# Kernel tuning notes

Hardware: AMD Instinct MI355X
Metric: run time of the kernel (lower is better)

## Reference

```python
import jax, jax.numpy as jnp
import numpy as np

N_NODES = 50000
N_EDGES = 800000
IN_F = 128
OUT_F = 32
HEADS = 4
EDGE_F = 32  # must equal OUT_F for the original module's shapes to broadcast


def setup_inputs() -> dict:
    key = jax.random.key(0)
    k1, k2, k3, k4, k5, k6, k7 = jax.random.split(key, 7)
    h = jax.random.normal(k1, (N_NODES, IN_F), dtype=jnp.float32)
    edge_indices = jax.random.randint(k2, (2, N_EDGES), 0, N_NODES, dtype=jnp.int32)
    edge_attr = jax.random.normal(k3, (N_EDGES, EDGE_F), dtype=jnp.float32)
    # learned parameters (xavier-ish scaling)
    W = jax.random.normal(k4, (IN_F, HEADS * OUT_F), dtype=jnp.float32) * (1.0 / np.sqrt(IN_F))
    a = jax.random.normal(k5, (HEADS, 2 * OUT_F + EDGE_F), dtype=jnp.float32) * 0.1
    eW = jax.random.normal(k6, (EDGE_F, HEADS * OUT_F), dtype=jnp.float32) * (1.0 / np.sqrt(EDGE_F))
    eb = jnp.zeros((HEADS * OUT_F,), dtype=jnp.float32)
    return {"h": h, "edge_indices": edge_indices, "edge_attr": edge_attr,
            "W": W, "a": a, "eW": eW, "eb": eb}


def reference(h, edge_indices, edge_attr, W, a, eW, eb):
    N = h.shape[0]
    H = a.shape[0]
    F = W.shape[1] // H
    row, col = edge_indices[0], edge_indices[1]

    # node / edge projections
    ht = (h @ W).reshape(N, H, F)                       # [N,H,F]
    et = (edge_attr @ eW + eb).reshape(-1, H, F)        # [E,H,F]

    # split attention vector; avoids materializing the [E,H,3F] concat
    a_i, a_j, a_e = a[:, :F], a[:, F:2 * F], a[:, 2 * F:]
    alpha_i = jnp.einsum('nhf,hf->nh', ht, a_i)         # [N,H]
    alpha_j = jnp.einsum('nhf,hf->nh', ht, a_j)         # [N,H]
    e = alpha_i[row] + alpha_j[col] + jnp.einsum('ehf,hf->eh', et, a_e)  # [E,H]
    e = jax.nn.leaky_relu(e, negative_slope=0.2)

    # scatter-softmax over edges grouped by destination (row), global-max stabilized
    e_exp = jnp.exp(e - jnp.max(e))                     # matches torch exp(e - e.max())
    denom = jax.ops.segment_sum(e_exp, row, num_segments=N)  # [N,H]
    att = e_exp / (denom[row] + 1e-8)                   # [E,H]

    # weighted scatter-add aggregation
    hj = ht[col]                                        # [E,H,F]
    h_out = jax.ops.segment_sum(att[:, :, None] * hj, row, num_segments=N)  # [N,H,F]
    h_out = h_out.reshape(N, H * F)                     # concat=True
    h_out = jax.nn.elu(h_out)                           # dropout=0 (eval)
    return h_out, att
```

## Files before the change

### kernel.cpp

```cpp
#include <hip/hip_runtime.h>
#include <hip/hip_bf16.h>
#include <hip/hip_fp16.h>

#define N_NODES 50000
#define N_EDGES 800000
#define IN_F 128
#define OUT_F 32
#define HEADS 4
#define EDGE_F 32
#define HF 128
#define SB 256
#define NBLK ((N_NODES + SB - 1) / SB)

typedef __attribute__((ext_vector_type(8))) short short8_t;
typedef __attribute__((ext_vector_type(4))) float f32x4;

__device__ __forceinline__ unsigned short f2bf(float x) {
    unsigned int u = __float_as_uint(x);
    unsigned int r = (u + 0x7FFF + ((u >> 16) & 1)) >> 16;
    return (unsigned short)r;
}
__device__ __forceinline__ float bf2f(unsigned short b) {
    return __uint_as_float(((unsigned int)b) << 16);
}

__global__ void prep_kernel(const float* __restrict__ eW, const float* __restrict__ eb,
                            const float* __restrict__ a,
                            float* __restrict__ w_eff, float* __restrict__ b_eff) {
    int t = threadIdx.x;
    if (t < 128) {
        int k = t >> 2, h = t & 3;
        float s = 0.f;
        #pragma unroll
        for (int f = 0; f < EDGE_F; ++f)
            s = fmaf(eW[k * HF + h * OUT_F + f], a[h * 96 + 2 * OUT_F + f], s);
        w_eff[k * 4 + h] = s;
    } else if (t < 132) {
        int h = t - 128;
        float s = 0.f;
        #pragma unroll
        for (int f = 0; f < EDGE_F; ++f)
            s = fmaf(eb[h * OUT_F + f], a[h * 96 + 2 * OUT_F + f], s);
        b_eff[h] = s;
    }
}

__global__ __launch_bounds__(256) void prepW_kernel(const float* __restrict__ W,
                                                    unsigned short* __restrict__ W_T) {
    int g = blockIdx.x * 256 + threadIdx.x;
    int n = g >> 4, c = g & 15;
    unsigned short w8[8];
    #pragma unroll
    for (int q = 0; q < 8; ++q)
        w8[q] = f2bf(W[(size_t)(8 * c + q) * 128 + n]);
    *(uint4*)&W_T[n * 128 + ((c ^ (n & 7)) << 3)] = *(uint4*)w8;
}

__global__ __launch_bounds__(256) void node_kernel(
        const float* __restrict__ h, const unsigned short* __restrict__ W_T,
        const float* __restrict__ a,
        __hip_bfloat16* __restrict__ ht_bf,
        float* __restrict__ alpha_i, float* __restrict__ alpha_j) {
    __shared__ __align__(16) unsigned short Wl[128 * 128];
    __shared__ __align__(16) unsigned short Hhi[64 * 128];
    __shared__ __align__(16) unsigned short Hlo[64 * 128];
    int t = threadIdx.x;
    int lane = t & 63, wave = t >> 6;
    int nb = blockIdx.x * 64;
    {
        const uint4* src = (const uint4*)W_T;
        uint4* dst = (uint4*)Wl;
        #pragma unroll
        for (int u = 0; u < 8; ++u) dst[t + u * 256] = src[t + u * 256];
    }
    #pragma unroll
    for (int u = 0; u < 8; ++u) {
        int f = u * 256 + t;
        int row = f >> 5, q = f & 31;
        int gn = nb + row; if (gn > N_NODES - 1) gn = N_NODES - 1;
        float4 v = ((const float4*)h)[(size_t)gn * 32 + q];
        unsigned short hi[4], lo[4];
        #pragma unroll
        for (int x = 0; x < 4; ++x) {
            float xv = (&v.x)[x];
            unsigned short hb = f2bf(xv);
            hi[x] = hb;
            lo[x] = f2bf(xv - bf2f(hb));
        }
        int c = q >> 1, half = q & 1;
        int off = row * 128 + ((c ^ (row & 7)) << 3) + half * 4;
        *(uint2*)&Hhi[off] = *(uint2*)hi;
        *(uint2*)&Hlo[off] = *(uint2*)lo;
    }
    __syncthreads();
    int n0 = nb + wave * 16;
    if (n0 >= N_NODES) return;
    int r = lane & 15, g = lane >> 4;
    short8_t ahi[4], alo[4];
    #pragma unroll
    for (int k = 0; k < 4; ++k) {
        int c = k * 4 + g;
        int off = (wave * 16 + r) * 128 + ((c ^ (r & 7)) << 3);
        ahi[k] = *(const short8_t*)&Hhi[off];
        alo[k] = *(const short8_t*)&Hlo[off];
    }
    f32x4 acc[8];
    #pragma unroll
    for (int i = 0; i < 8; ++i) acc[i] = (f32x4){0.f, 0.f, 0.f, 0.f};
    #pragma unroll
    for (int tt = 0; tt < 8; ++tt) {
        int n = tt * 16 + r;
        #pragma unroll
        for (int k = 0; k < 4; ++k) {
            int c = k * 4 + g;
            short8_t b = *(const short8_t*)&Wl[n * 128 + ((c ^ (n & 7)) << 3)];
            acc[tt] = __builtin_amdgcn_mfma_f32_16x16x32_bf16(ahi[k], b, acc[tt], 0, 0, 0);
            acc[tt] = __builtin_amdgcn_mfma_f32_16x16x32_bf16(alo[k], b, acc[tt], 0, 0, 0);
        }
    }
    #pragma unroll
    for (int tt = 0; tt < 8; ++tt)
        #pragma unroll
        for (int reg = 0; reg < 4; ++reg) {
            int rowg = n0 + 4 * g + reg;
            ((unsigned short*)ht_bf)[(size_t)rowg * 128 + tt * 16 + r] = f2bf(acc[tt][reg]);
        }
    float pi[4][4], pj[4][4];
    #pragma unroll
    for (int hh = 0; hh < 4; ++hh) {
        float ai0 = a[hh * 96 + r],      ai1 = a[hh * 96 + 16 + r];
        float aj0 = a[hh * 96 + 32 + r], aj1 = a[hh * 96 + 48 + r];
        #pragma unroll
        for (int reg = 0; reg < 4; ++reg) {
            float v0 = acc[2 * hh][reg], v1 = acc[2 * hh + 1][reg];
            pi[hh][reg] = fmaf(v0, ai0, v1 * ai1);
            pj[hh][reg] = fmaf(v0, aj0, v1 * aj1);
        }
    }
    #pragma unroll
    for (int hh = 0; hh < 4; ++hh)
        #pragma unroll
        for (int reg = 0; reg < 4; ++reg) {
            float vi = pi[hh][reg], vj = pj[hh][reg];
            #pragma unroll
            for (int s = 1; s < 16; s <<= 1) {
                vi += __shfl_xor(vi, s, 64);
                vj += __shfl_xor(vj, s, 64);
            }
            pi[hh][reg] = vi; pj[hh][reg] = vj;
        }
    if (r == 0) {
        #pragma unroll
        for (int hh = 0; hh < 4; ++hh)
            #pragma unroll
            for (int reg = 0; reg < 4; ++reg) {
                int rowg = n0 + 4 * g + reg;
                alpha_i[rowg * 4 + hh] = pi[hh][reg];
                alpha_j[rowg * 4 + hh] = pj[hh][reg];
            }
    }
}

__global__ __launch_bounds__(256) void count_kernel(const int* __restrict__ row,
                                                    int* __restrict__ deg,
                                                    int* __restrict__ rank) {
    int t = blockIdx.x * 256 + threadIdx.x;
    if (t < N_EDGES / 4) {
        int4 r4 = ((const int4*)row)[t];
        int4 k4;
        k4.x = atomicAdd(&deg[r4.x], 1);
        k4.y = atomicAdd(&deg[r4.y], 1);
        k4.z = atomicAdd(&deg[r4.z], 1);
        k4.w = atomicAdd(&deg[r4.w], 1);
        ((int4*)rank)[t] = k4;
    }
}

__device__ __forceinline__ int block_incl_scan(int v, int lane, int wid, int* wsum) {
    int x = v;
    #pragma unroll
    for (int s = 1; s < 64; s <<= 1) {
        int y = __shfl_up(x, s, 64);
        if (lane >= s) x += y;
    }
    if (lane == 63) wsum[wid] = x;
    __syncthreads();
    int add = 0;
    #pragma unroll
    for (int w = 0; w < 4; ++w) add += (w < wid) ? wsum[w] : 0;
    return x + add;
}

__global__ __launch_bounds__(SB) void scan1_kernel(const int* __restrict__ deg,
                                                   int* __restrict__ row_off,
                                                   int* __restrict__ blk_sums) {
    __shared__ int wsum[4];
    int i = blockIdx.x * SB + threadIdx.x;
    int v = (i < N_NODES) ? deg[i] : 0;
    int incl = block_incl_scan(v, threadIdx.x & 63, threadIdx.x >> 6, wsum);
    if (i < N_NODES) row_off[i] = incl - v;
    if (threadIdx.x == SB - 1) blk_sums[blockIdx.x] = incl;
}

__global__ __launch_bounds__(SB) void scan2_kernel(int* __restrict__ blk_sums,
                                                   int* __restrict__ blk_off,
                                                   int* __restrict__ row_off) {
    __shared__ int wsum[4];
    int t = threadIdx.x;
    int v = (t < NBLK) ? blk_sums[t] : 0;
    int incl = block_incl_scan(v, t & 63, t >> 6, wsum);
    if (t < NBLK) blk_off[t] = incl - v;
    if (t == SB - 1) row_off[N_NODES] = incl;
}

__global__ __launch_bounds__(SB) void scan3_kernel(const int* __restrict__ blk_off,
                                                   int* __restrict__ row_off,
                                                   const float* __restrict__ alpha_i,
                                                   float4* __restrict__ nrec) {
    int i = blockIdx.x * SB + threadIdx.x;
    if (i < N_NODES) {
        int v = row_off[i] + blk_off[blockIdx.x];
        row_off[i] = v;
        float4 ai = *(const float4*)(alpha_i + (size_t)i * 4);
        nrec[(size_t)i * 2] = ai;
        float4 m;
        m.x = __int_as_float(v); m.y = 0.f; m.z = 0.f; m.w = 0.f;
        nrec[(size_t)i * 2 + 1] = m;
    }
}

__global__ __launch_bounds__(256) void edge_kernel(
        const int* __restrict__ row, const int* __restrict__ col,
        const int* __restrict__ rank,
        const float* __restrict__ ea,
        const float* __restrict__ w_eff, const float* __restrict__ b_eff,
        const float4* __restrict__ nrec, const float* __restrict__ alpha_j,
        uint4* __restrict__ rec, float4* __restrict__ att_ex) {
    __shared__ __align__(16) float eas[256 * 36];
    __shared__ float wsd[128];
    __shared__ float bs[4];
    int t = threadIdx.x;
    if (t < 128) wsd[t] = w_eff[t];
    if (t < 4) bs[t] = b_eff[t];
    int e0 = blockIdx.x * 256;
    {
        const float4* src = (const float4*)ea + (size_t)e0 * 8;
        #pragma unroll
        for (int u = 0; u < 8; ++u) {
            int f = u * 256 + t;
            int el = f >> 3, j = f & 7;
            *(float4*)&eas[el * 36 + 4 * j] = src[f];
        }
    }
    __syncthreads();
    int e = e0 + t;
    float4 ev[8];
    #pragma unroll
    for (int i = 0; i < 8; ++i) ev[i] = *(const float4*)&eas[t * 36 + 4 * i];
    int r = row[e], c = col[e];
    int rk = rank[e];
    f32x4 ai = ((const f32x4*)nrec)[(size_t)r * 2];
    int ro = ((const int*)nrec)[(size_t)r * 8 + 4];
    f32x4 aj = *(const f32x4*)(alpha_j + (size_t)c * 4);
    float s0 = bs[0], s1 = bs[1], s2 = bs[2], s3 = bs[3];
    #pragma unroll
    for (int i = 0; i < 8; ++i) {
        #pragma unroll
        for (int kk = 0; kk < 4; ++kk) {
            float x = (&ev[i].x)[kk];
            float4 w4 = *(const float4*)&wsd[(i * 4 + kk) * 4];
            s0 = fmaf(x, w4.x, s0);
            s1 = fmaf(x, w4.y, s1);
            s2 = fmaf(x, w4.z, s2);
            s3 = fmaf(x, w4.w, s3);
        }
    }
    float e0v = s0 + ai[0] + aj[0];
    float e1v = s1 + ai[1] + aj[1];
    float e2v = s2 + ai[2] + aj[2];
    float e3v = s3 + ai[3] + aj[3];
    e0v = e0v > 0.f ? e0v : 0.2f * e0v;
    e1v = e1v > 0.f ? e1v : 0.2f * e1v;
    e2v = e2v > 0.f ? e2v : 0.2f * e2v;
    e3v = e3v > 0.f ? e3v : 0.2f * e3v;
    float x0 = __expf(e0v), x1 = __expf(e1v), x2 = __expf(e2v), x3 = __expf(e3v);
    att_ex[e] = make_float4(x0, x1, x2, x3);
    __half2 p01 = __floats2half2_rn(x0, x1);
    __half2 p23 = __floats2half2_rn(x2, x3);
    uint4 o;
    o.x = *reinterpret_cast<unsigned int*>(&p01);
    o.y = *reinterpret_cast<unsigned int*>(&p23);
    o.z = (unsigned int)c;
    o.w = 0u;
    rec[ro + rk] = o;
}

__global__ __launch_bounds__(256) void agg_kernel(
        const int* __restrict__ row_off, const uint4* __restrict__ rec,
        const __hip_bfloat16* __restrict__ ht_bf,
        float* __restrict__ hout, float* __restrict__ rden_buf) {
    int wave = threadIdx.x >> 6;
    int lane = threadIdx.x & 63;
    int n = blockIdx.x * 4 + wave;
    if (n >= N_NODES) return;
    int beg = row_off[n], end = row_off[n + 1];
    int h2 = lane >> 4;
    int sh = (h2 & 1) * 16;
    float2 acc0 = {0.f, 0.f}, acc1 = {0.f, 0.f};
    float den0 = 0.f, den1 = 0.f;
    int p = beg;
    for (; p + 3 < end; p += 4) {
        uint4 rA = rec[p];
        uint4 rB = rec[p + 1];
        uint4 rC = rec[p + 2];
        uint4 rD = rec[p + 3];
        unsigned int wA = (h2 & 2) ? rA.y : rA.x;
        unsigned int wB = (h2 & 2) ? rB.y : rB.x;
        unsigned int wC = (h2 & 2) ? rC.y : rC.x;
        unsigned int wD = (h2 & 2) ? rD.y : rD.x;
        float exA = __half2float(__ushort_as_half((unsigned short)(wA >> sh)));
        float exB = __half2float(__ushort_as_half((unsigned short)(wB >> sh)));
        float exC = __half2float(__ushort_as_half((unsigned short)(wC >> sh)));
        float exD = __half2float(__ushort_as_half((unsigned short)(wD >> sh)));
        float2 hvA = __bfloat1622float2(
            *(const __hip_bfloat162*)(ht_bf + (size_t)rA.z * HF + 2 * lane));
        float2 hvB = __bfloat1622float2(
            *(const __hip_bfloat162*)(ht_bf + (size_t)rB.z * HF + 2 * lane));
        float2 hvC = __bfloat1622float2(
            *(const __hip_bfloat162*)(ht_bf + (size_t)rC.z * HF + 2 * lane));
        float2 hvD = __bfloat1622float2(
            *(const __hip_bfloat162*)(ht_bf + (size_t)rD.z * HF + 2 * lane));
        acc0.x = fmaf(exA, hvA.x, acc0.x); acc0.y = fmaf(exA, hvA.y, acc0.y);
        acc1.x = fmaf(exB, hvB.x, acc1.x); acc1.y = fmaf(exB, hvB.y, acc1.y);
        acc0.x = fmaf(exC, hvC.x, acc0.x); acc0.y = fmaf(exC, hvC.y, acc0.y);
        acc1.x = fmaf(exD, hvD.x, acc1.x); acc1.y = fmaf(exD, hvD.y, acc1.y);
        den0 += exA + exC; den1 += exB + exD;
    }
    for (; p < end; ++p) {
        uint4 rA = rec[p];
        unsigned int wA = (h2 & 2) ? rA.y : rA.x;
        float exA = __half2float(__ushort_as_half((unsigned short)(wA >> sh)));
        float2 hvA = __bfloat1622float2(
            *(const __hip_bfloat162*)(ht_bf + (size_t)rA.z * HF + 2 * lane));
        acc0.x = fmaf(exA, hvA.x, acc0.x); acc0.y = fmaf(exA, hvA.y, acc0.y);
        den0 += exA;
    }
    float den = den0 + den1;
    float rden = 1.0f / (den + 1e-8f);
    float ox = (acc0.x + acc1.x) * rden, oy = (acc0.y + acc1.y) * rden;
    ox = ox > 0.f ? ox : expm1f(ox);
    oy = oy > 0.f ? oy : expm1f(oy);
    float2 o = {ox, oy};
    ((float2*)(hout + (size_t)n * HF))[lane] = o;
    if ((lane & 15) == 0)
        rden_buf[n * 4 + h2] = rden;
}

__global__ __launch_bounds__(256) void norm_kernel(const int* __restrict__ row,
                                                   const float* __restrict__ rden_buf,
                                                   float* __restrict__ att) {
    int e = blockIdx.x * 256 + threadIdx.x;
    float4 ex = ((const float4*)att)[e];
    int r = row[e];
    float4 rd = *(const float4*)(rden_buf + (size_t)r * 4);
    ex.x *= rd.x; ex.y *= rd.y; ex.z *= rd.z; ex.w *= rd.w;
    ((float4*)att)[e] = ex;
}

extern "C" void kernel_launch(void* const* d_in, const int* in_sizes, int n_in,
                              void* d_out, int out_size, void* d_ws, size_t ws_size,
                              hipStream_t stream) {
    const float* h  = (const float*)d_in[0];
    const int*   ei = (const int*)  d_in[1];
    const float* ea = (const float*)d_in[2];
    const float* W  = (const float*)d_in[3];
    const float* a  = (const float*)d_in[4];
    const float* eW = (const float*)d_in[5];
    const float* eb = (const float*)d_in[6];

    float* out  = (float*)d_out;
    float* hout = out;
    float* att  = out + (size_t)N_NODES * HF;

    char* wsb = (char*)d_ws;
    __hip_bfloat16* ht_bf = (__hip_bfloat16*)wsb;
    float* alpha_i = (float*)(wsb + (size_t)N_NODES * HF * 2);
    float* alpha_j = alpha_i + N_NODES * HEADS;
    float* w_eff   = alpha_j + N_NODES * HEADS;
    float* b_eff   = w_eff + 128;
    unsigned short* W_T = (unsigned short*)(b_eff + 4);
    int*   deg     = (int*)(W_T + 128 * 128);
    int*   row_off = deg + N_NODES;
    int*   blk_sums= row_off + N_NODES + 1;
    int*   blk_off = blk_sums + NBLK;
    int*   rank    = (int*)((((uintptr_t)(blk_off + NBLK)) + 15) & ~(uintptr_t)15);
    uint4* rec     = (uint4*)((((uintptr_t)(rank + N_EDGES)) + 15) & ~(uintptr_t)15);
    float* rden_buf= (float*)(rec + N_EDGES);
    float4* nrec   = (float4*)(rden_buf + N_NODES * 4);

    const int* row = ei;
    const int* col = ei + N_EDGES;

    (void)hipMemsetAsync(deg, 0, (size_t)N_NODES * sizeof(int), stream);

    prep_kernel<<<1, 160, 0, stream>>>(eW, eb, a, w_eff, b_eff);
    prepW_kernel<<<8, 256, 0, stream>>>(W, W_T);
    node_kernel<<<(N_NODES + 63) / 64, 256, 0, stream>>>(h, W_T, a, ht_bf, alpha_i, alpha_j);
    count_kernel<<<(N_EDGES / 4 + 255) / 256, 256, 0, stream>>>(row, deg, rank);
    scan1_kernel<<<NBLK, SB, 0, stream>>>(deg, row_off, blk_sums);
    scan2_kernel<<<1, SB, 0, stream>>>(blk_sums, blk_off, row_off);
    scan3_kernel<<<NBLK, SB, 0, stream>>>(blk_off, row_off, alpha_i, nrec);
    edge_kernel<<<N_EDGES / 256, 256, 0, stream>>>(row, col, rank, ea, w_eff, b_eff,
                                                   nrec, alpha_j, rec, (float4*)att);
    agg_kernel<<<(N_NODES + 3) / 4, 256, 0, stream>>>(row_off, rec, ht_bf, hout, rden_buf);
    norm_kernel<<<N_EDGES / 256, 256, 0, stream>>>(row, rden_buf, att);
}
```

Baseline: 329.0 us.

## Merge prep kernels, fuse degree count into node kernel, unroll agg by 8

```diff
diff --git a/kernel.cpp b/kernel.cpp
--- a/kernel.cpp
+++ b/kernel.cpp
@@ -11,6 +11,8 @@
 #define HF 128
 #define SB 256
 #define NBLK ((N_NODES + SB - 1) / SB)
+#define NODE_BLKS ((N_NODES + 63) / 64)
+#define CNT_BLKS ((N_EDGES / 4 + 255) / 256)
 
 typedef __attribute__((ext_vector_type(8))) short short8_t;
 typedef __attribute__((ext_vector_type(4))) float f32x4;
@@ -24,47 +26,63 @@
     return __uint_as_float(((unsigned int)b) << 16);
 }
 
-__global__ void prep_kernel(const float* __restrict__ eW, const float* __restrict__ eb,
-                            const float* __restrict__ a,
-                            float* __restrict__ w_eff, float* __restrict__ b_eff) {
+__global__ __launch_bounds__(256) void prep_kernel(
+        const float* __restrict__ W, const float* __restrict__ eW,
+        const float* __restrict__ eb, const float* __restrict__ a,
+        unsigned short* __restrict__ W_T,
+        float* __restrict__ w_eff, float* __restrict__ b_eff) {
     int t = threadIdx.x;
-    if (t < 128) {
-        int k = t >> 2, h = t & 3;
-        float s = 0.f;
-        #pragma unroll
-        for (int f = 0; f < EDGE_F; ++f)
-            s = fmaf(eW[k * HF + h * OUT_F + f], a[h * 96 + 2 * OUT_F + f], s);
-        w_eff[k * 4 + h] = s;
-    } else if (t < 132) {
-        int h = t - 128;
-        float s = 0.f;
-        #pragma unroll
-        for (int f = 0; f < EDGE_F; ++f)
-            s = fmaf(eb[h * OUT_F + f], a[h * 96 + 2 * OUT_F + f], s);
-        b_eff[h] = s;
-    }
-}
-
-__global__ __launch_bounds__(256) void prepW_kernel(const float* __restrict__ W,
-                                                    unsigned short* __restrict__ W_T) {
-    int g = blockIdx.x * 256 + threadIdx.x;
-    int n = g >> 4, c = g & 15;
-    unsigned short w8[8];
-    #pragma unroll
-    for (int q = 0; q < 8; ++q)
-        w8[q] = f2bf(W[(size_t)(8 * c + q) * 128 + n]);
-    *(uint4*)&W_T[n * 128 + ((c ^ (n & 7)) << 3)] = *(uint4*)w8;
-}
-
-__global__ __launch_bounds__(256) void node_kernel(
+    if (blockIdx.x < 8) {
+        int g = blockIdx.x * 256 + t;
+        int n = g >> 4, c = g & 15;
+        unsigned short w8[8];
+        #pragma unroll
+        for (int q = 0; q < 8; ++q)
+            w8[q] = f2bf(W[(size_t)(8 * c + q) * 128 + n]);
+        *(uint4*)&W_T[n * 128 + ((c ^ (n & 7)) << 3)] = *(uint4*)w8;
+    } else {
+        if (t < 128) {
+            int k = t >> 2, h = t & 3;
+            float s = 0.f;
+            #pragma unroll
+            for (int f = 0; f < EDGE_F; ++f)
+                s = fmaf(eW[k * HF + h * OUT_F + f], a[h * 96 + 2 * OUT_F + f], s);
+            w_eff[k * 4 + h] = s;
+        } else if (t < 132) {
+            int h = t - 128;
+            float s = 0.f;
+            #pragma unroll
+            for (int f = 0; f < EDGE_F; ++f)
+                s = fmaf(eb[h * OUT_F + f], a[h * 96 + 2 * OUT_F + f], s);
+            b_eff[h] = s;
+        }
+    }
+}
+
+__global__ __launch_bounds__(256) void node_count_kernel(
         const float* __restrict__ h, const unsigned short* __restrict__ W_T,
         const float* __restrict__ a,
         __hip_bfloat16* __restrict__ ht_bf,
-        float* __restrict__ alpha_i, float* __restrict__ alpha_j) {
+        float* __restrict__ alpha_i, float* __restrict__ alpha_j,
+        const int* __restrict__ row, int* __restrict__ deg,
+        int* __restrict__ rank) {
     __shared__ __align__(16) unsigned short Wl[128 * 128];
     __shared__ __align__(16) unsigned short Hhi[64 * 128];
     __shared__ __align__(16) unsigned short Hlo[64 * 128];
     int t = threadIdx.x;
+    if (blockIdx.x >= NODE_BLKS) {
+        int i = (blockIdx.x - NODE_BLKS) * 256 + t;
+        if (i < N_EDGES / 4) {
+            int4 r4 = ((const int4*)row)[i];
+            int4 k4;
+            k4.x = atomicAdd(&deg[r4.x], 1);
+            k4.y = atomicAdd(&deg[r4.y], 1);
+            k4.z = atomicAdd(&deg[r4.z], 1);
+            k4.w = atomicAdd(&deg[r4.w], 1);
+            ((int4*)rank)[i] = k4;
+        }
+        return;
+    }
     int lane = t & 63, wave = t >> 6;
     int nb = blockIdx.x * 64;
     {
@@ -76,8 +94,8 @@
     #pragma unroll
     for (int u = 0; u < 8; ++u) {
         int f = u * 256 + t;
-        int row = f >> 5, q = f & 31;
-        int gn = nb + row; if (gn > N_NODES - 1) gn = N_NODES - 1;
+        int r_ = f >> 5, q = f & 31;
+        int gn = nb + r_; if (gn > N_NODES - 1) gn = N_NODES - 1;
         float4 v = ((const float4*)h)[(size_t)gn * 32 + q];
         unsigned short hi[4], lo[4];
         #pragma unroll
@@ -88,7 +106,7 @@
             lo[x] = f2bf(xv - bf2f(hb));
         }
         int c = q >> 1, half = q & 1;
-        int off = row * 128 + ((c ^ (row & 7)) << 3) + half * 4;
+        int off = r_ * 128 + ((c ^ (r_ & 7)) << 3) + half * 4;
         *(uint2*)&Hhi[off] = *(uint2*)hi;
         *(uint2*)&Hlo[off] = *(uint2*)lo;
     }
@@ -158,21 +176,6 @@
                 alpha_i[rowg * 4 + hh] = pi[hh][reg];
                 alpha_j[rowg * 4 + hh] = pj[hh][reg];
             }
-    }
-}
-
-__global__ __launch_bounds__(256) void count_kernel(const int* __restrict__ row,
-                                                    int* __restrict__ deg,
-                                                    int* __restrict__ rank) {
-    int t = blockIdx.x * 256 + threadIdx.x;
-    if (t < N_EDGES / 4) {
-        int4 r4 = ((const int4*)row)[t];
-        int4 k4;
-        k4.x = atomicAdd(&deg[r4.x], 1);
-        k4.y = atomicAdd(&deg[r4.y], 1);
-        k4.z = atomicAdd(&deg[r4.z], 1);
-        k4.w = atomicAdd(&deg[r4.w], 1);
-        ((int4*)rank)[t] = k4;
     }
 }
 
@@ -309,32 +312,29 @@
     float2 acc0 = {0.f, 0.f}, acc1 = {0.f, 0.f};
     float den0 = 0.f, den1 = 0.f;
     int p = beg;
-    for (; p + 3 < end; p += 4) {
-        uint4 rA = rec[p];
-        uint4 rB = rec[p + 1];
-        uint4 rC = rec[p + 2];
-        uint4 rD = rec[p + 3];
-        unsigned int wA = (h2 & 2) ? rA.y : rA.x;
-        unsigned int wB = (h2 & 2) ? rB.y : rB.x;
-        unsigned int wC = (h2 & 2) ? rC.y : rC.x;
-        unsigned int wD = (h2 & 2) ? rD.y : rD.x;
-        float exA = __half2float(__ushort_as_half((unsigned short)(wA >> sh)));
-        float exB = __half2float(__ushort_as_half((unsigned short)(wB >> sh)));
-        float exC = __half2float(__ushort_as_half((unsigned short)(wC >> sh)));
-        float exD = __half2float(__ushort_as_half((unsigned short)(wD >> sh)));
-        float2 hvA = __bfloat1622float2(
-            *(const __hip_bfloat162*)(ht_bf + (size_t)rA.z * HF + 2 * lane));
-        float2 hvB = __bfloat1622float2(
-            *(const __hip_bfloat162*)(ht_bf + (size_t)rB.z * HF + 2 * lane));
-        float2 hvC = __bfloat1622float2(
-            *(const __hip_bfloat162*)(ht_bf + (size_t)rC.z * HF + 2 * lane));
-        float2 hvD = __bfloat1622float2(
-            *(const __hip_bfloat162*)(ht_bf + (size_t)rD.z * HF + 2 * lane));
-        acc0.x = fmaf(exA, hvA.x, acc0.x); acc0.y = fmaf(exA, hvA.y, acc0.y);
-        acc1.x = fmaf(exB, hvB.x, acc1.x); acc1.y = fmaf(exB, hvB.y, acc1.y);
-        acc0.x = fmaf(exC, hvC.x, acc0.x); acc0.y = fmaf(exC, hvC.y, acc0.y);
-        acc1.x = fmaf(exD, hvD.x, acc1.x); acc1.y = fmaf(exD, hvD.y, acc1.y);
-        den0 += exA + exC; den1 += exB + exD;
+    for (; p + 7 < end; p += 8) {
+        uint4 rr[8];
+        #pragma unroll
+        for (int u = 0; u < 8; ++u) rr[u] = rec[p + u];
+        float ex[8];
+        #pragma unroll
+        for (int u = 0; u < 8; ++u) {
+            unsigned int w = (h2 & 2) ? rr[u].y : rr[u].x;
+            ex[u] = __half2float(__ushort_as_half((unsigned short)(w >> sh)));
+        }
+        float2 hv[8];
+        #pragma unroll
+        for (int u = 0; u < 8; ++u)
+            hv[u] = __bfloat1622float2(
+                *(const __hip_bfloat162*)(ht_bf + (size_t)rr[u].z * HF + 2 * lane));
+        #pragma unroll
+        for (int u = 0; u < 8; u += 2) {
+            acc0.x = fmaf(ex[u], hv[u].x, acc0.x);
+            acc0.y = fmaf(ex[u], hv[u].y, acc0.y);
+            acc1.x = fmaf(ex[u + 1], hv[u + 1].x, acc1.x);
+            acc1.y = fmaf(ex[u + 1], hv[u + 1].y, acc1.y);
+            den0 += ex[u]; den1 += ex[u + 1];
+        }
     }
     for (; p < end; ++p) {
         uint4 rA = rec[p];
@@ -403,15 +403,14 @@
 
     (void)hipMemsetAsync(deg, 0, (size_t)N_NODES * sizeof(int), stream);
 
-    prep_kernel<<<1, 160, 0, stream>>>(eW, eb, a, w_eff, b_eff);
-    prepW_kernel<<<8, 256, 0, stream>>>(W, W_T);
-    node_kernel<<<(N_NODES + 63) / 64, 256, 0, stream>>>(h, W_T, a, ht_bf, alpha_i, alpha_j);
-    count_kernel<<<(N_EDGES / 4 + 255) / 256, 256, 0, stream>>>(row, deg, rank);
+    prep_kernel<<<9, 256, 0, stream>>>(W, eW, eb, a, W_T, w_eff, b_eff);
+    node_count_kernel<<<NODE_BLKS + CNT_BLKS, 256, 0, stream>>>(
+        h, W_T, a, ht_bf, alpha_i, alpha_j, row, deg, rank);
     scan1_kernel<<<NBLK, SB, 0, stream>>>(deg, row_off, blk_sums);
     scan2_kernel<<<1, SB, 0, stream>>>(blk_sums, blk_off, row_off);
     scan3_kernel<<<NBLK, SB, 0, stream>>>(blk_off, row_off, alpha_i, nrec);
     edge_kernel<<<N_EDGES / 256, 256, 0, stream>>>(row, col, rank, ea, w_eff, b_eff,
                                                    nrec, alpha_j, rec, (float4*)att);
     agg_kernel<<<(N_NODES + 3) / 4, 256, 0, stream>>>(row_off, rec, ht_bf, hout, rden_buf);
-    norm_kernel<<<N_EDGES / 256, 256, 0, stream>>>(row, rden_buf, att);
-}
+    norm_kernel<<<N_EDGES / 256, 0 ? 0 : 256, 0, stream>>>(row, rden_buf, att);
+}
```

New measurement: 426.3 us. 1.3x slower.
